# Optimization experiments

Hardware: AMD Instinct MI355X
Metric: run time of the kernel (lower is better)

The kernel has to match this reference:

```python
import jax, jax.numpy as jnp
import numpy as np

N, C, T, V = 16, 128, 128, 25
K, H, OC = 3, 8, 256          # kernel_size subsets, heads, out_channels
HOPMAX = 12                   # hop values in [0, 12); emb_table size HOPMAX
EPS_BN = 1e-5
EPS_NORM = 1e-4


def setup_inputs() -> dict:
    key = jax.random.key(0)
    ks = jax.random.split(key, 12)
    s = 0.05
    x = jax.random.normal(ks[0], (N, C, T, V), jnp.float32)
    hop = jax.random.randint(ks[1], (V, V), 0, HOPMAX)
    emb_table = jax.random.normal(ks[2], (K, H, HOPMAX), jnp.float32) * s
    # A initialized as identity (as in the module) plus small noise for nontrivial grads
    A = jnp.tile(jnp.eye(V, dtype=jnp.float32), (K, H, 1, 1)) \
        + jax.random.normal(ks[3], (K, H, V, V), jnp.float32) * s
    w_block = jax.random.normal(ks[4], (K * OC, C // H), jnp.float32) * s  # grouped 1x1 conv, groups=K*H
    b_block = jax.random.normal(ks[5], (K * OC,), jnp.float32) * s
    bn_gamma = jnp.ones((OC,), jnp.float32)
    bn_beta = jnp.zeros((OC,), jnp.float32)
    res_w = jax.random.normal(ks[6], (OC, C), jnp.float32) * s  # residual 1x1 conv
    res_b = jax.random.normal(ks[7], (OC,), jnp.float32) * s
    res_bn_gamma = jnp.ones((OC,), jnp.float32)
    res_bn_beta = jnp.zeros((OC,), jnp.float32)
    return {"x": x, "hop": hop, "emb_table": emb_table, "A": A,
            "w_block": w_block, "b_block": b_block,
            "bn_gamma": bn_gamma, "bn_beta": bn_beta,
            "res_w": res_w, "res_b": res_b,
            "res_bn_gamma": res_bn_gamma, "res_bn_beta": res_bn_beta}


def _batchnorm(x, gamma, beta):
    # training-mode BatchNorm2d: batch stats over (N, T, V), biased variance
    m = jnp.mean(x, axis=(0, 2, 3), keepdims=True)
    v = jnp.var(x, axis=(0, 2, 3), keepdims=True)
    xn = (x - m) * jax.lax.rsqrt(v + EPS_BN)
    return gamma[None, :, None, None] * xn + beta[None, :, None, None]


def _l2_col_norm(w):
    # torch.norm(w, p=2, dim=-2, keepdim=True) + 1e-4  (in-degree normalization)
    return jnp.sqrt(jnp.sum(w * w, axis=-2, keepdims=True)) + EPS_NORM


def reference(x, hop, emb_table, A, w_block, b_block, bn_gamma, bn_beta,
              res_w, res_b, res_bn_gamma, res_bn_beta):
    n, c, t, v = x.shape
    # residual: 1x1 TemporalConv2d + BN (in_channels != out_channels)
    res = jnp.einsum('nctv,oc->notv', x, res_w) + res_b[None, :, None, None]
    res = _batchnorm(res, res_bn_gamma, res_bn_beta)

    # hop-embedding gather -> [K, H, V, V]; fuse normalized B and A
    B = emb_table[:, :, hop]
    BnA = B / _l2_col_norm(B) + A / _l2_col_norm(A)

    # graph conv: einsum over joint dim v (broadcast over k)
    xh = x.reshape(n, H, c // H, t, v)                      # [N,H,C/H,T,V]
    y = jnp.einsum('nhctv,khvw->nkhctw', xh, BnA)           # [N,K,H,C/H,T,V]
    y = y.reshape(n, K * H, c // H, t, v)                   # groups = K*H

    # grouped 1x1 conv: per-group [C/H -> OC/H] GEMM
    wg = w_block.reshape(K * H, OC // H, c // H)
    out = jnp.einsum('ngctv,goc->ngotv', y, wg)             # [N,K*H,OC/H,T,V]
    out = out.reshape(n, K * OC, t, v) + b_block[None, :, None, None]

    # sum over the K kernel subsets
    out = out.reshape(n, K, OC, t, v).sum(axis=1)
    out = _batchnorm(out, bn_gamma, bn_beta)
    return jax.nn.relu(out + res)
```

## Files before the change

kernel.cpp:

```cpp
#include <hip/hip_runtime.h>
#include <stdint.h>

typedef __attribute__((ext_vector_type(8))) short short8;
typedef __attribute__((ext_vector_type(4))) float f32x4;

#define B_BNA    0ull
#define B_STATS  60416ull
#define B_RESW2  64512ull
#define B_PART   130048ull
#define B_E2     1178624ull
#define B_XB     7994368ull
#define B_MAIN   21625856ull
#define B_RES    47840256ull

#define NTV 51200.0f

__device__ __forceinline__ unsigned short f2bf(float f) {
    unsigned u = __float_as_uint(f);
    return (unsigned short)((u + 0x7fffu + ((u >> 16) & 1u)) >> 16);
}
__device__ __forceinline__ float bf2f(unsigned s) { return __uint_as_float(s << 16); }

__device__ __forceinline__ float wave_sum(float v) {
#pragma unroll
    for (int m = 1; m < 64; m <<= 1) v += __shfl_xor(v, m, 64);
    return v;
}

__global__ __launch_bounds__(256) void k_prep(const int* __restrict__ hop,
                                              const float* __restrict__ emb,
                                              const float* __restrict__ A,
                                              const float* __restrict__ res_w,
                                              float* __restrict__ bna,
                                              float* __restrict__ stats,
                                              unsigned short* __restrict__ resw2) {
    int g = blockIdx.x, tid = threadIdx.x;
    if (g < 24) {
        if (tid < 25) {
            int w = tid;
            float nb = 0.f, na = 0.f;
            for (int v = 0; v < 25; v++) {
                float e = emb[g*12 + hop[v*25 + w]];
                nb += e*e;
                float a = A[((size_t)g*25 + v)*25 + w];
                na += a*a;
            }
            nb = sqrtf(nb) + 1e-4f;
            na = sqrtf(na) + 1e-4f;
            for (int v = 0; v < 25; v++) {
                float e = emb[g*12 + hop[v*25 + w]];
                float a = A[((size_t)g*25 + v)*25 + w];
                bna[g*625 + v*25 + w] = e/nb + a/na;
            }
        }
    } else if (g == 24) {
#pragma unroll
        for (int i = 0; i < 4; i++) stats[i*256 + tid] = 0.f;
    } else {
        int base = (g - 25) * 4096 + tid * 16;
#pragma unroll
        for (int j = 0; j < 16; j++) resw2[base + j] = f2bf(res_w[base + j]);
    }
}

__global__ __launch_bounds__(256) void k_prep2(const float* __restrict__ w_block,
                                               const float* __restrict__ bna,
                                               unsigned short* __restrict__ E2) {
    __shared__ float bl[3*625];
    __shared__ float wl[3*64];
    int bid = blockIdx.x;
    int half = bid & 1, og = (bid >> 1) & 7, h = bid >> 4;
    int tid = threadIdx.x;

    for (int i = tid; i < 1875; i += 256) {
        int k3 = i / 625, j = i - k3*625;
        bl[i] = bna[(k3*8 + h)*625 + j];
    }
    if (tid < 192) {
        int k3 = tid >> 6, o = (tid >> 4) & 3, c = tid & 15;
        wl[tid] = w_block[(k3*256 + h*32 + og*4 + o)*16 + c];
    }
    __syncthreads();

    unsigned short* dst = E2 + (size_t)(h*8 + og)*53248;
    int e0 = half * 26624;
    for (int e = e0 + tid; e < e0 + 26624; e += 256) {
        int kc = e >> 12;
        int n  = (e >> 5) & 127;
        int kk = e & 31;
        int k  = kc*32 + kk;
        int o  = n >> 5, w = n & 31;
        float val = 0.f;
        if (k < 400 && w < 25) {
            int c = k / 25, v = k - c*25;
            val = wl[0*64 + o*16 + c] * bl[0*625 + v*25 + w]
                + wl[1*64 + o*16 + c] * bl[1*625 + v*25 + w]
                + wl[2*64 + o*16 + c] * bl[2*625 + v*25 + w];
        }
        dst[e] = f2bf(val);
    }
}

__global__ __launch_bounds__(256) void k_xprep(const float* __restrict__ x,
                                               unsigned short* __restrict__ xb) {
    int b = blockIdx.x;
    int n_ = b >> 7, t_ = b & 127;
    int tid = threadIdx.x;
    unsigned short* row = xb + (size_t)b * 3328;
    for (int idx = tid; idx < 3200; idx += 256) {
        int c = idx / 25, v = idx - c*25;
        float val = x[(((size_t)n_*128 + c)*128 + t_)*25 + v];
        row[(c >> 4)*416 + (c & 15)*25 + v] = f2bf(val);
    }
    if (tid < 128) row[(tid >> 4)*416 + 400 + (tid & 15)] = 0;
}

__global__ __launch_bounds__(256) void k_gc(const unsigned short* __restrict__ xb,
                                            const unsigned short* __restrict__ E2,
                                            unsigned short* __restrict__ mainp,
                                            float* __restrict__ stats) {
    __shared__ unsigned short Alds[128*32];
    __shared__ unsigned short Blds[128*32];
    int bid = blockIdx.x;
    int og = bid & 7, h = (bid >> 3) & 7, mt = bid >> 6;
    int tid = threadIdx.x;
    int lane = tid & 63, wave = tid >> 6;
    int wm = wave >> 1, wn = wave & 1;
    int lane15 = lane & 15, quad = lane >> 4;

    int srow = tid >> 1, shalf = tid & 1;
    const size_t abase = (size_t)(mt*128 + srow)*3328 + h*416 + shalf*16;
    const size_t bchunk0 = (size_t)(((h*8 + og)*13))*4096 + tid*16;

    f32x4 acc[4][4] = {};

    for (int kc = 0; kc < 13; kc++) {
        {
            const uint4* s = (const uint4*)(xb + abase + kc*32);
            uint4 a0 = s[0], a1 = s[1];
            *(uint4*)&Alds[srow*32 + shalf*16]     = a0;
            *(uint4*)&Alds[srow*32 + shalf*16 + 8] = a1;
        }
        {
            const uint4* s = (const uint4*)(E2 + bchunk0 + (size_t)kc*4096);
            uint4 b0 = s[0], b1 = s[1];
            *(uint4*)&Blds[tid*16]     = b0;
            *(uint4*)&Blds[tid*16 + 8] = b1;
        }
        __syncthreads();

        short8 af[4], bf[4];
#pragma unroll
        for (int i = 0; i < 4; i++) {
            af[i] = *(const short8*)&Alds[(wm*64 + i*16 + lane15)*32 + quad*8];
            bf[i] = *(const short8*)&Blds[(wn*64 + i*16 + lane15)*32 + quad*8];
        }
#pragma unroll
        for (int i = 0; i < 4; i++)
#pragma unroll
            for (int j = 0; j < 4; j++)
                acc[i][j] = __builtin_amdgcn_mfma_f32_16x16x32_bf16(af[i], bf[j], acc[i][j], 0, 0, 0);
        __syncthreads();
    }

    float s1[2] = {0.f, 0.f}, s2[2] = {0.f, 0.f};
#pragma unroll
    for (int j = 0; j < 4; j++) {
        int w = (j & 1)*16 + lane15;
        int p = j >> 1;
        if (w < 25) {
            int oc = h*32 + og*4 + wn*2 + p;
#pragma unroll
            for (int i = 0; i < 4; i++) {
                int mb = mt*128 + wm*64 + i*16 + quad*4;
#pragma unroll
                for (int r = 0; r < 4; r++) {
                    float val = acc[i][j][r];
                    mainp[(size_t)((mb + r)*256 + oc)*25 + w] = f2bf(val);
                    s1[p] += val;
                    s2[p] = fmaf(val, val, s2[p]);
                }
            }
        }
    }
#pragma unroll
    for (int p = 0; p < 2; p++) {
        float a = wave_sum(s1[p]);
        float b = wave_sum(s2[p]);
        if (lane == 0) {
            int oc = h*32 + og*4 + wn*2 + p;
            atomicAdd(&stats[oc], a);
            atomicAdd(&stats[256 + oc], b);
        }
    }
}

__global__ __launch_bounds__(256) void k_res(const float* __restrict__ x,
                                             const unsigned short* __restrict__ resw2,
                                             unsigned short* __restrict__ resp,
                                             float* __restrict__ stats) {
    __shared__ unsigned short Alds[128*32];
    __shared__ unsigned short Blds[128*32];
    int bid = blockIdx.x;
    int nt = bid & 1, mt = bid >> 1;
    int tid = threadIdx.x;
    int lane = tid & 63, wave = tid >> 6;
    int wm = wave >> 1, wn = wave & 1;
    int lane15 = lane & 15, quad = lane >> 4;

    int m2row = tid >> 1, shalf = tid & 1;
    int m2 = mt*128 + m2row;
    int bb = m2 / 25, vv = m2 - bb*25;
    int n_ = bb >> 7, t_ = bb & 127;
    const float* xbase = x + ((size_t)n_*128*128 + t_)*25 + vv;

    f32x4 acc[4][4] = {};

    for (int kc = 0; kc < 4; kc++) {
        {
            unsigned short tmp[16];
            int c0 = kc*32 + shalf*16;
#pragma unroll
            for (int j = 0; j < 16; j++)
                tmp[j] = f2bf(xbase[(size_t)(c0 + j)*3200]);
            unsigned pk[8];
#pragma unroll
            for (int q = 0; q < 8; q++)
                pk[q] = (unsigned)tmp[2*q] | ((unsigned)tmp[2*q+1] << 16);
            *(uint4*)&Alds[m2row*32 + shalf*16]     = make_uint4(pk[0], pk[1], pk[2], pk[3]);
            *(uint4*)&Alds[m2row*32 + shalf*16 + 8] = make_uint4(pk[4], pk[5], pk[6], pk[7]);
        }
        {
            const uint4* s = (const uint4*)(resw2 + (size_t)(nt*128 + m2row)*128 + kc*32 + shalf*16);
            uint4 b0 = s[0], b1 = s[1];
            *(uint4*)&Blds[m2row*32 + shalf*16]     = b0;
            *(uint4*)&Blds[m2row*32 + shalf*16 + 8] = b1;
        }
        __syncthreads();

        short8 af[4], bf[4];
#pragma unroll
        for (int i = 0; i < 4; i++) {
            af[i] = *(const short8*)&Alds[(wm*64 + i*16 + lane15)*32 + quad*8];
            bf[i] = *(const short8*)&Blds[(wn*64 + i*16 + lane15)*32 + quad*8];
        }
#pragma unroll
        for (int i = 0; i < 4; i++)
#pragma unroll
            for (int j = 0; j < 4; j++)
                acc[i][j] = __builtin_amdgcn_mfma_f32_16x16x32_bf16(af[i], bf[j], acc[i][j], 0, 0, 0);
        __syncthreads();
    }

#pragma unroll
    for (int j = 0; j < 4; j++) {
        int oc = nt*128 + wn*64 + j*16 + lane15;
        float s1 = 0.f, s2 = 0.f;
#pragma unroll
        for (int i = 0; i < 4; i++) {
            int m2b = mt*128 + wm*64 + i*16 + quad*4;
#pragma unroll
            for (int r = 0; r < 4; r++) {
                float val = acc[i][j][r];
                int m2e = m2b + r;
                int b = m2e / 25, v = m2e - b*25;
                resp[(size_t)(b*256 + oc)*25 + v] = f2bf(val);
                s1 += val;
                s2 = fmaf(val, val, s2);
            }
        }
        s1 += __shfl_xor(s1, 16, 64); s1 += __shfl_xor(s1, 32, 64);
        s2 += __shfl_xor(s2, 16, 64); s2 += __shfl_xor(s2, 32, 64);
        if (quad == 0) {
            atomicAdd(&stats[512 + oc], s1);
            atomicAdd(&stats[768 + oc], s2);
        }
    }
}

__global__ __launch_bounds__(256) void k_final(const float* __restrict__ bn_g,
                                               const float* __restrict__ bn_b,
                                               const float* __restrict__ rbn_g,
                                               const float* __restrict__ rbn_b,
                                               const float* __restrict__ stats,
                                               const unsigned short* __restrict__ mainp,
                                               const unsigned short* __restrict__ resp,
                                               float* __restrict__ out) {
    int b = blockIdx.x;
    int n_ = b >> 7, t_ = b & 127;
    int oc = threadIdx.x;
    const float inv = 1.f / NTV;
    float s1 = stats[oc],       s2 = stats[256 + oc];
    float r1 = stats[512 + oc], r2 = stats[768 + oc];
    float mm = s1*inv, vm = s2*inv - mm*mm;
    float mr = r1*inv, vr = r2*inv - mr*mr;
    float a1 = bn_g[oc]  * rsqrtf(vm + 1e-5f); float c1 = bn_b[oc]  - a1*mm;
    float a2 = rbn_g[oc] * rsqrtf(vr + 1e-5f); float c2 = rbn_b[oc] - a2*mr;

    const unsigned short* mrow = mainp + (size_t)(b*256 + oc)*25;
    const unsigned short* rrow = resp  + (size_t)(b*256 + oc)*25;
    float* op = out + ((size_t)(n_*256 + oc)*128 + t_)*25;
#pragma unroll
    for (int w = 0; w < 25; w++) {
        float val = fmaf(a1, bf2f(mrow[w]), c1) + fmaf(a2, bf2f(rrow[w]), c2);
        op[w] = fmaxf(val, 0.f);
    }
}

extern "C" void kernel_launch(void* const* d_in, const int* in_sizes, int n_in,
                              void* d_out, int out_size, void* d_ws, size_t ws_size,
                              hipStream_t stream) {
    const float* x        = (const float*)d_in[0];
    const int*   hop      = (const int*)  d_in[1];
    const float* emb      = (const float*)d_in[2];
    const float* A        = (const float*)d_in[3];
    const float* w_block  = (const float*)d_in[4];
    const float* bn_g     = (const float*)d_in[6];
    const float* bn_b     = (const float*)d_in[7];
    const float* res_w    = (const float*)d_in[8];
    const float* rbn_g    = (const float*)d_in[10];
    const float* rbn_b    = (const float*)d_in[11];
    float* out = (float*)d_out;

    char* ws = (char*)d_ws;
    float*          bna    = (float*)(ws + B_BNA);
    float*          stats  = (float*)(ws + B_STATS);
    unsigned short* resw2  = (unsigned short*)(ws + B_RESW2);
    unsigned short* E2     = (unsigned short*)(ws + B_E2);
    unsigned short* xb     = (unsigned short*)(ws + B_XB);
    unsigned short* mainp  = (unsigned short*)(ws + B_MAIN);
    unsigned short* resp   = (unsigned short*)(ws + B_RES);

    k_prep  <<<33,   256, 0, stream>>>(hop, emb, A, res_w, bna, stats, resw2);
    k_prep2 <<<128,  256, 0, stream>>>(w_block, bna, E2);
    k_xprep <<<2048, 256, 0, stream>>>(x, xb);
    k_gc    <<<1024, 256, 0, stream>>>(xb, E2, mainp, stats);
    k_res   <<<800,  256, 0, stream>>>(x, resw2, resp, stats);
    k_final <<<2048, 256, 0, stream>>>(bn_g, bn_b, rbn_g, rbn_b, stats, mainp, resp, out);
}
```

Baseline: 240.8 us.

## Merge prep kernels, fuse residual GEMM with x conversion, double-buffer graph-conv GEMM

The six-kernel pipeline becomes four launches. BnA normalization is folded into the E2 weight build, and residual weight conversion moves inline. The x bf16 conversion and the residual GEMM share one launch, and the residual GEMM is transposed so x loads are coalesced float4 reads instead of strided scalar loads. The graph-conv GEMM gains double-buffered LDS with padded rows to overlap global loads with MFMA and cut bank conflicts. The final BN/ReLU kernel stages the main and residual tiles through LDS with vector loads. The tradeoff is more LDS per block and some redundant prep work across blocks.

```diff
diff --git a/kernel.cpp b/kernel.cpp
--- a/kernel.cpp
+++ b/kernel.cpp
@@ -4,10 +4,7 @@
 typedef __attribute__((ext_vector_type(8))) short short8;
 typedef __attribute__((ext_vector_type(4))) float f32x4;
 
-#define B_BNA    0ull
 #define B_STATS  60416ull
-#define B_RESW2  64512ull
-#define B_PART   130048ull
 #define B_E2     1178624ull
 #define B_XB     7994368ull
 #define B_MAIN   21625856ull
@@ -27,58 +24,47 @@
     return v;
 }
 
-__global__ __launch_bounds__(256) void k_prep(const int* __restrict__ hop,
-                                              const float* __restrict__ emb,
-                                              const float* __restrict__ A,
-                                              const float* __restrict__ res_w,
-                                              float* __restrict__ bna,
-                                              float* __restrict__ stats,
-                                              unsigned short* __restrict__ resw2) {
-    int g = blockIdx.x, tid = threadIdx.x;
-    if (g < 24) {
-        if (tid < 25) {
-            int w = tid;
-            float nb = 0.f, na = 0.f;
-            for (int v = 0; v < 25; v++) {
-                float e = emb[g*12 + hop[v*25 + w]];
-                nb += e*e;
-                float a = A[((size_t)g*25 + v)*25 + w];
-                na += a*a;
-            }
-            nb = sqrtf(nb) + 1e-4f;
-            na = sqrtf(na) + 1e-4f;
-            for (int v = 0; v < 25; v++) {
-                float e = emb[g*12 + hop[v*25 + w]];
-                float a = A[((size_t)g*25 + v)*25 + w];
-                bna[g*625 + v*25 + w] = e/nb + a/na;
-            }
-        }
-    } else if (g == 24) {
+__global__ __launch_bounds__(256) void k_prepE(const int* __restrict__ hop,
+                                               const float* __restrict__ emb,
+                                               const float* __restrict__ A,
+                                               const float* __restrict__ w_block,
+                                               unsigned short* __restrict__ E2,
+                                               float* __restrict__ stats) {
+    int bid = blockIdx.x, tid = threadIdx.x;
+    if (bid == 128) {
 #pragma unroll
         for (int i = 0; i < 4; i++) stats[i*256 + tid] = 0.f;
-    } else {
-        int base = (g - 25) * 4096 + tid * 16;
-#pragma unroll
-        for (int j = 0; j < 16; j++) resw2[base + j] = f2bf(res_w[base + j]);
-    }
-}
-
-__global__ __launch_bounds__(256) void k_prep2(const float* __restrict__ w_block,
-                                               const float* __restrict__ bna,
-                                               unsigned short* __restrict__ E2) {
-    __shared__ float bl[3*625];
-    __shared__ float wl[3*64];
-    int bid = blockIdx.x;
+        return;
+    }
+    __shared__ float bl[1875];
+    __shared__ float wl[192];
+    __shared__ float invn[150];
     int half = bid & 1, og = (bid >> 1) & 7, h = bid >> 4;
-    int tid = threadIdx.x;
-
-    for (int i = tid; i < 1875; i += 256) {
-        int k3 = i / 625, j = i - k3*625;
-        bl[i] = bna[(k3*8 + h)*625 + j];
+
+    if (tid < 75) {
+        int k3 = tid / 25, w = tid - k3*25;
+        int g = k3*8 + h;
+        float nb = 0.f, na = 0.f;
+        for (int v = 0; v < 25; v++) {
+            float e = emb[g*12 + hop[v*25 + w]];
+            nb += e*e;
+            float a = A[((size_t)g*25 + v)*25 + w];
+            na += a*a;
+        }
+        invn[tid]      = 1.f / (sqrtf(nb) + 1e-4f);
+        invn[75 + tid] = 1.f / (sqrtf(na) + 1e-4f);
     }
     if (tid < 192) {
         int k3 = tid >> 6, o = (tid >> 4) & 3, c = tid & 15;
         wl[tid] = w_block[(k3*256 + h*32 + og*4 + o)*16 + c];
+    }
+    __syncthreads();
+    for (int i = tid; i < 1875; i += 256) {
+        int k3 = i / 625, vw = i - k3*625, v = vw / 25, w = vw - v*25;
+        int g = k3*8 + h;
+        float e = emb[g*12 + hop[v*25 + w]];
+        float a = A[((size_t)g*25 + v)*25 + w];
+        bl[i] = e*invn[k3*25 + w] + a*invn[75 + k3*25 + w];
     }
     __syncthreads();
 
@@ -101,28 +87,124 @@
     }
 }
 
-__global__ __launch_bounds__(256) void k_xprep(const float* __restrict__ x,
-                                               unsigned short* __restrict__ xb) {
-    int b = blockIdx.x;
-    int n_ = b >> 7, t_ = b & 127;
-    int tid = threadIdx.x;
-    unsigned short* row = xb + (size_t)b * 3328;
-    for (int idx = tid; idx < 3200; idx += 256) {
-        int c = idx / 25, v = idx - c*25;
-        float val = x[(((size_t)n_*128 + c)*128 + t_)*25 + v];
-        row[(c >> 4)*416 + (c & 15)*25 + v] = f2bf(val);
-    }
-    if (tid < 128) row[(tid >> 4)*416 + 400 + (tid & 15)] = 0;
+__global__ __launch_bounds__(256) void k_xres(const float* __restrict__ x,
+                                              const float* __restrict__ res_w,
+                                              unsigned short* __restrict__ xb,
+                                              unsigned short* __restrict__ resp,
+                                              float* __restrict__ stats) {
+    __shared__ unsigned short Al[128*40];
+    __shared__ unsigned short Bl[128*40];
+    int bid = blockIdx.x, tid = threadIdx.x;
+
+    if (bid < 2048) {
+        int n_ = bid >> 7, t_ = bid & 127;
+        unsigned short* row = xb + (size_t)bid * 3328;
+        for (int idx = tid; idx < 3200; idx += 256) {
+            int c = idx / 25, v = idx - c*25;
+            float val = x[(((size_t)n_*128 + c)*128 + t_)*25 + v];
+            row[(c >> 4)*416 + (c & 15)*25 + v] = f2bf(val);
+        }
+        if (tid < 128) row[(tid >> 4)*416 + 400 + (tid & 15)] = 0;
+        return;
+    }
+
+    int rid = bid - 2048;
+    int nt = rid & 1, mt = rid >> 1;
+    int lane = tid & 63, wave = tid >> 6;
+    int wm = wave >> 1, wn = wave & 1;
+    int lane15 = lane & 15, quad = lane >> 4;
+
+    int srow = tid >> 1, shalf = tid & 1;
+    int m2grp = tid & 31, ckk = tid >> 5;
+    int n_ = mt / 25;
+    int rembase = (mt - n_*25)*128 + m2grp*4;
+    const float* xn = x + (size_t)n_*128*3200;
+
+    f32x4 acc[4][4] = {};
+
+    for (int kc = 0; kc < 4; kc++) {
+        {
+            const float4* s = (const float4*)(res_w + (size_t)(nt*128 + srow)*128 + kc*32 + shalf*16);
+            float4 f0 = s[0], f1 = s[1], f2 = s[2], f3 = s[3];
+            float fv[16] = {f0.x,f0.y,f0.z,f0.w, f1.x,f1.y,f1.z,f1.w,
+                            f2.x,f2.y,f2.z,f2.w, f3.x,f3.y,f3.z,f3.w};
+            unsigned pk[8];
+#pragma unroll
+            for (int q = 0; q < 8; q++)
+                pk[q] = (unsigned)f2bf(fv[2*q]) | ((unsigned)f2bf(fv[2*q+1]) << 16);
+            *(uint4*)&Al[srow*40 + shalf*16]     = make_uint4(pk[0],pk[1],pk[2],pk[3]);
+            *(uint4*)&Al[srow*40 + shalf*16 + 8] = make_uint4(pk[4],pk[5],pk[6],pk[7]);
+        }
+        {
+            float4 xv[4];
+#pragma unroll
+            for (int dk = 0; dk < 4; dk++) {
+                int c = kc*32 + ckk*4 + dk;
+                xv[dk] = *(const float4*)(xn + (size_t)c*3200 + rembase);
+            }
+#pragma unroll
+            for (int r = 0; r < 4; r++) {
+                float b0 = (r==0?xv[0].x:r==1?xv[0].y:r==2?xv[0].z:xv[0].w);
+                float b1 = (r==0?xv[1].x:r==1?xv[1].y:r==2?xv[1].z:xv[1].w);
+                float b2 = (r==0?xv[2].x:r==1?xv[2].y:r==2?xv[2].z:xv[2].w);
+                float b3 = (r==0?xv[3].x:r==1?xv[3].y:r==2?xv[3].z:xv[3].w);
+                unsigned p0 = (unsigned)f2bf(b0) | ((unsigned)f2bf(b1) << 16);
+                unsigned p1 = (unsigned)f2bf(b2) | ((unsigned)f2bf(b3) << 16);
+                *(uint2*)&Bl[(m2grp*4 + r)*40 + ckk*4] = make_uint2(p0, p1);
+            }
+        }
+        __syncthreads();
+
+        short8 af[4], bf[4];
+#pragma unroll
+        for (int i = 0; i < 4; i++) {
+            af[i] = *(const short8*)&Al[(wm*64 + i*16 + lane15)*40 + quad*8];
+            bf[i] = *(const short8*)&Bl[(wn*64 + i*16 + lane15)*40 + quad*8];
+        }
+#pragma unroll
+        for (int i = 0; i < 4; i++)
+#pragma unroll
+            for (int j = 0; j < 4; j++)
+                acc[i][j] = __builtin_amdgcn_mfma_f32_16x16x32_bf16(af[i], bf[j], acc[i][j], 0, 0, 0);
+        __syncthreads();
+    }
+
+#pragma unroll
+    for (int i = 0; i < 4; i++) {
+#pragma unroll
+        for (int r = 0; r < 4; r++) {
+            int oc = nt*128 + wm*64 + i*16 + quad*4 + r;
+            float sv = 0.f, sq = 0.f;
+#pragma unroll
+            for (int j = 0; j < 4; j++) {
+                float val = acc[i][j][r];
+                int M2 = mt*128 + wn*64 + j*16 + lane15;
+                int b = M2 / 25, v = M2 - b*25;
+                resp[(size_t)(b*256 + oc)*25 + v] = f2bf(val);
+                sv += val;
+                sq = fmaf(val, val, sq);
+            }
+            sv += __shfl_xor(sv, 1, 64); sv += __shfl_xor(sv, 2, 64);
+            sv += __shfl_xor(sv, 4, 64); sv += __shfl_xor(sv, 8, 64);
+            sq += __shfl_xor(sq, 1, 64); sq += __shfl_xor(sq, 2, 64);
+            sq += __shfl_xor(sq, 4, 64); sq += __shfl_xor(sq, 8, 64);
+            if (lane15 == 0) {
+                atomicAdd(&stats[512 + oc], sv);
+                atomicAdd(&stats[768 + oc], sq);
+            }
+        }
+    }
 }
 
 __global__ __launch_bounds__(256) void k_gc(const unsigned short* __restrict__ xb,
                                             const unsigned short* __restrict__ E2,
                                             unsigned short* __restrict__ mainp,
                                             float* __restrict__ stats) {
-    __shared__ unsigned short Alds[128*32];
-    __shared__ unsigned short Blds[128*32];
+    __shared__ unsigned short Al[2][128*40];
+    __shared__ unsigned short Bl[2][128*40];
     int bid = blockIdx.x;
-    int og = bid & 7, h = (bid >> 3) & 7, mt = bid >> 6;
+    int mt = bid & 15, hog = bid >> 4;
+    int h = hog >> 3, og = hog & 7;
     int tid = threadIdx.x;
     int lane = tid & 63, wave = tid >> 6;
     int wm = wave >> 1, wn = wave & 1;
@@ -130,36 +212,46 @@
 
     int srow = tid >> 1, shalf = tid & 1;
     const size_t abase = (size_t)(mt*128 + srow)*3328 + h*416 + shalf*16;
-    const size_t bchunk0 = (size_t)(((h*8 + og)*13))*4096 + tid*16;
+    const size_t bbase = (size_t)hog*53248 + tid*16;
+    int sof = srow*40 + shalf*16;
+
+    {
+        const uint4* sa = (const uint4*)(xb + abase);
+        uint4 a0 = sa[0], a1 = sa[1];
+        *(uint4*)&Al[0][sof] = a0; *(uint4*)&Al[0][sof + 8] = a1;
+        const uint4* sb = (const uint4*)(E2 + bbase);
+        uint4 b0 = sb[0], b1 = sb[1];
+        *(uint4*)&Bl[0][sof] = b0; *(uint4*)&Bl[0][sof + 8] = b1;
+    }
+    __syncthreads();
 
     f32x4 acc[4][4] = {};
 
     for (int kc = 0; kc < 13; kc++) {
-        {
-            const uint4* s = (const uint4*)(xb + abase + kc*32);
-            uint4 a0 = s[0], a1 = s[1];
-            *(uint4*)&Alds[srow*32 + shalf*16]     = a0;
-            *(uint4*)&Alds[srow*32 + shalf*16 + 8] = a1;
-        }
-        {
-            const uint4* s = (const uint4*)(E2 + bchunk0 + (size_t)kc*4096);
-            uint4 b0 = s[0], b1 = s[1];
-            *(uint4*)&Blds[tid*16]     = b0;
-            *(uint4*)&Blds[tid*16 + 8] = b1;
-        }
-        __syncthreads();
-
+        int cur = kc & 1, nxt = cur ^ 1;
+        uint4 a0, a1, b0, b1;
+        bool hasNext = (kc < 12);
+        if (hasNext) {
+            const uint4* sa = (const uint4*)(xb + abase + (kc + 1)*32);
+            a0 = sa[0]; a1 = sa[1];
+            const uint4* sb = (const uint4*)(E2 + bbase + (size_t)(kc + 1)*4096);
+            b0 = sb[0]; b1 = sb[1];
+        }
         short8 af[4], bf[4];
 #pragma unroll
         for (int i = 0; i < 4; i++) {
-            af[i] = *(const short8*)&Alds[(wm*64 + i*16 + lane15)*32 + quad*8];
-            bf[i] = *(const short8*)&Blds[(wn*64 + i*16 + lane15)*32 + quad*8];
+            af[i] = *(const short8*)&Al[cur][(wm*64 + i*16 + lane15)*40 + quad*8];
+            bf[i] = *(const short8*)&Bl[cur][(wn*64 + i*16 + lane15)*40 + quad*8];
         }
 #pragma unroll
         for (int i = 0; i < 4; i++)
 #pragma unroll
             for (int j = 0; j < 4; j++)
                 acc[i][j] = __builtin_amdgcn_mfma_f32_16x16x32_bf16(af[i], bf[j], acc[i][j], 0, 0, 0);
+        if (hasNext) {
+            *(uint4*)&Al[nxt][sof] = a0; *(uint4*)&Al[nxt][sof + 8] = a1;
+            *(uint4*)&Bl[nxt][sof] = b0; *(uint4*)&Bl[nxt][sof + 8] = b1;
+        }
         __syncthreads();
     }
 
@@ -191,89 +283,6 @@
             int oc = h*32 + og*4 + wn*2 + p;
             atomicAdd(&stats[oc], a);
             atomicAdd(&stats[256 + oc], b);
-        }
-    }
-}
-
-__global__ __launch_bounds__(256) void k_res(const float* __restrict__ x,
-                                             const unsigned short* __restrict__ resw2,
-                                             unsigned short* __restrict__ resp,
-                                             float* __restrict__ stats) {
-    __shared__ unsigned short Alds[128*32];
-    __shared__ unsigned short Blds[128*32];
-    int bid = blockIdx.x;
-    int nt = bid & 1, mt = bid >> 1;
-    int tid = threadIdx.x;
-    int lane = tid & 63, wave = tid >> 6;
-    int wm = wave >> 1, wn = wave & 1;
-    int lane15 = lane & 15, quad = lane >> 4;
-
-    int m2row = tid >> 1, shalf = tid & 1;
-    int m2 = mt*128 + m2row;
-    int bb = m2 / 25, vv = m2 - bb*25;
-    int n_ = bb >> 7, t_ = bb & 127;
-    const float* xbase = x + ((size_t)n_*128*128 + t_)*25 + vv;
-
-    f32x4 acc[4][4] = {};
-
-    for (int kc = 0; kc < 4; kc++) {
-        {
-            unsigned short tmp[16];
-            int c0 = kc*32 + shalf*16;
-#pragma unroll
-            for (int j = 0; j < 16; j++)
-                tmp[j] = f2bf(xbase[(size_t)(c0 + j)*3200]);
-            unsigned pk[8];
-#pragma unroll
-            for (int q = 0; q < 8; q++)
-                pk[q] = (unsigned)tmp[2*q] | ((unsigned)tmp[2*q+1] << 16);
-            *(uint4*)&Alds[m2row*32 + shalf*16]     = make_uint4(pk[0], pk[1], pk[2], pk[3]);
-            *(uint4*)&Alds[m2row*32 + shalf*16 + 8] = make_uint4(pk[4], pk[5], pk[6], pk[7]);
-        }
-        {
-            const uint4* s = (const uint4*)(resw2 + (size_t)(nt*128 + m2row)*128 + kc*32 + shalf*16);
-            uint4 b0 = s[0], b1 = s[1];
-            *(uint4*)&Blds[m2row*32 + shalf*16]     = b0;
-            *(uint4*)&Blds[m2row*32 + shalf*16 + 8] = b1;
-        }
-        __syncthreads();
-
-        short8 af[4], bf[4];
-#pragma unroll
-        for (int i = 0; i < 4; i++) {
-            af[i] = *(const short8*)&Alds[(wm*64 + i*16 + lane15)*32 + quad*8];
-            bf[i] = *(const short8*)&Blds[(wn*64 + i*16 + lane15)*32 + quad*8];
-        }
-#pragma unroll
-        for (int i = 0; i < 4; i++)
-#pragma unroll
-            for (int j = 0; j < 4; j++)
-                acc[i][j] = __builtin_amdgcn_mfma_f32_16x16x32_bf16(af[i], bf[j], acc[i][j], 0, 0, 0);
-        __syncthreads();
-    }
-
-#pragma unroll
-    for (int j = 0; j < 4; j++) {
-        int oc = nt*128 + wn*64 + j*16 + lane15;
-        float s1 = 0.f, s2 = 0.f;
-#pragma unroll
-        for (int i = 0; i < 4; i++) {
-            int m2b = mt*128 + wm*64 + i*16 + quad*4;
-#pragma unroll
-            for (int r = 0; r < 4; r++) {
-                float val = acc[i][j][r];
-                int m2e = m2b + r;
-                int b = m2e / 25, v = m2e - b*25;
-                resp[(size_t)(b*256 + oc)*25 + v] = f2bf(val);
-                s1 += val;
-                s2 = fmaf(val, val, s2);
-            }
-        }
-        s1 += __shfl_xor(s1, 16, 64); s1 += __shfl_xor(s1, 32, 64);
-        s2 += __shfl_xor(s2, 16, 64); s2 += __shfl_xor(s2, 32, 64);
-        if (quad == 0) {
-            atomicAdd(&stats[512 + oc], s1);
-            atomicAdd(&stats[768 + oc], s2);
         }
     }
 }
@@ -286,9 +295,21 @@
                                                const unsigned short* __restrict__ mainp,
                                                const unsigned short* __restrict__ resp,
                                                float* __restrict__ out) {
+    __shared__ unsigned short ml[6400];
+    __shared__ unsigned short rl[6400];
     int b = blockIdx.x;
     int n_ = b >> 7, t_ = b & 127;
-    int oc = threadIdx.x;
+    int tid = threadIdx.x;
+
+    const uint4* msrc = (const uint4*)(mainp + (size_t)b*6400);
+    const uint4* rsrc = (const uint4*)(resp  + (size_t)b*6400);
+    for (int idx = tid; idx < 800; idx += 256) {
+        ((uint4*)ml)[idx] = msrc[idx];
+        ((uint4*)rl)[idx] = rsrc[idx];
+    }
+    __syncthreads();
+
+    int oc = tid;
     const float inv = 1.f / NTV;
     float s1 = stats[oc],       s2 = stats[256 + oc];
     float r1 = stats[512 + oc], r2 = stats[768 + oc];
@@ -297,12 +318,10 @@
     float a1 = bn_g[oc]  * rsqrtf(vm + 1e-5f); float c1 = bn_b[oc]  - a1*mm;
     float a2 = rbn_g[oc] * rsqrtf(vr + 1e-5f); float c2 = rbn_b[oc] - a2*mr;
 
-    const unsigned short* mrow = mainp + (size_t)(b*256 + oc)*25;
-    const unsigned short* rrow = resp  + (size_t)(b*256 + oc)*25;
     float* op = out + ((size_t)(n_*256 + oc)*128 + t_)*25;
 #pragma unroll
     for (int w = 0; w < 25; w++) {
-        float val = fmaf(a1, bf2f(mrow[w]), c1) + fmaf(a2, bf2f(rrow[w]), c2);
+        float val = fmaf(a1, bf2f(ml[oc*25 + w]), c1) + fmaf(a2, bf2f(rl[oc*25 + w]), c2);
         op[w] = fmaxf(val, 0.f);
     }
 }
@@ -323,18 +342,14 @@
     float* out = (float*)d_out;
 
     char* ws = (char*)d_ws;
-    float*          bna    = (float*)(ws + B_BNA);
     float*          stats  = (float*)(ws + B_STATS);
-    unsigned short* resw2  = (unsigned short*)(ws + B_RESW2);
     unsigned short* E2     = (unsigned short*)(ws + B_E2);
     unsigned short* xb     = (unsigned short*)(ws + B_XB);
     unsigned short* mainp  = (unsigned short*)(ws + B_MAIN);
     unsigned short* resp   = (unsigned short*)(ws + B_RES);
 
-    k_prep  <<<33,   256, 0, stream>>>(hop, emb, A, res_w, bna, stats, resw2);
-    k_prep2 <<<128,  256, 0, stream>>>(w_block, bna, E2);
-    k_xprep <<<2048, 256, 0, stream>>>(x, xb);
+    k_prepE <<<129,  256, 0, stream>>>(hop, emb, A, w_block, E2, stats);
+    k_xres  <<<2848, 256, 0, stream>>>(x, res_w, xb, resp, stats);
     k_gc    <<<1024, 256, 0, stream>>>(xb, E2, mainp, stats);
-    k_res   <<<800,  256, 0, stream>>>(x, resw2, resp, stats);
     k_final <<<2048, 256, 0, stream>>>(bn_g, bn_b, rbn_g, rbn_b, stats, mainp, resp, out);
 }
```

Measured after the change: 307.2 us. 1.28x slower.
